# Kernel optimization log

Measured on AMD Instinct MI355X. Metric: run time of the kernel, lower is better.

The kernel has to match this reference:

```python
import jax, jax.numpy as jnp
import numpy as np

D_MODEL = 256   # per-head dim in this module
N_HEAD = 8
B, S = 4, 2048
NEG_INF = -1e9  # large negative in place of -inf for numerical safety


def setup_inputs() -> dict:
    key = jax.random.key(0)
    ks = jax.random.split(key, 8)
    d, h = D_MODEL, N_HEAD
    sc = 1.0 / np.sqrt(d)
    return {
        "Q": jax.random.normal(ks[0], (B, S, d), jnp.float32),
        "mask": jax.random.randint(ks[1], (B, S), 0, 2, jnp.int32),
        "WQ_w": jax.random.normal(ks[2], (h * d, d), jnp.float32) * sc,
        "WQ_b": jnp.zeros((h * d,), jnp.float32),
        "WK_w": jax.random.normal(ks[3], (h * d, d), jnp.float32) * sc,
        "WK_b": jnp.zeros((h * d,), jnp.float32),
        "WV_w": jax.random.normal(ks[4], (h * d, d), jnp.float32) * sc,
        "WV_b": jnp.zeros((h * d,), jnp.float32),
        "WO_w": jax.random.normal(ks[5], (d, h * d), jnp.float32) * sc,
        "WO_b": jnp.zeros((d,), jnp.float32),
        "ln_g": jnp.ones((d,), jnp.float32),
        "ln_b": jnp.zeros((d,), jnp.float32),
    }


def reference(Q, mask, WQ_w, WQ_b, WK_w, WK_b, WV_w, WV_b, WO_w, WO_b, ln_g, ln_b):
    b, s, d = Q.shape
    h = N_HEAD
    # projections (torch Linear: x @ W.T + b), split into heads: [b, h, s, d]
    q = (Q @ WQ_w.T + WQ_b).reshape(b, s, h, d).transpose(0, 2, 1, 3)
    k = (Q @ WK_w.T + WK_b).reshape(b, s, h, d).transpose(0, 2, 1, 3)
    v = (Q @ WV_w.T + WV_b).reshape(b, s, h, d).transpose(0, 2, 1, 3)
    # scaled dot-product scores [b, h, q, k]
    scores = jnp.einsum('bhqd,bhkd->bhqk', q, k) / jnp.sqrt(jnp.asarray(d, Q.dtype))
    key_mask = (mask != 0)[:, None, None, :]  # [b,1,1,k]
    scores = jnp.where(key_mask, scores, NEG_INF)
    alpha = jax.nn.softmax(scores, axis=-1)
    out = jnp.einsum('bhqk,bhkd->bhqd', alpha, v)
    out = out.transpose(0, 2, 1, 3).reshape(b, s, h * d)
    out = out @ WO_w.T + WO_b + Q  # dropout is identity in eval
    # LayerNorm over last dim
    mu = out.mean(-1, keepdims=True)
    var = out.var(-1, keepdims=True)
    return (out - mu) / jnp.sqrt(var + 1e-5) * ln_g + ln_b
```

## Files before the change

kernel.cpp:

```cpp
#include <hip/hip_runtime.h>
#include <cstddef>
#include <cstdint>

#define SQ 2048
#define DH 256
#define NH 8
#define BATCH 4
#define MROWS (BATCH*SQ)
#define HID (NH*DH)

typedef __attribute__((ext_vector_type(8)))  short bf16x8;
typedef __attribute__((ext_vector_type(16))) float f32x16;

typedef __attribute__((address_space(1))) const unsigned char gbuf_t;
typedef __attribute__((address_space(3))) unsigned char lbuf_t;

__device__ __forceinline__ void gl_lds16(const void* g, void* l) {
  __builtin_amdgcn_global_load_lds((gbuf_t*)g, (lbuf_t*)l, 16, 0, 0);
}

__device__ __forceinline__ unsigned short f2bf(float f) {
  unsigned u = __float_as_uint(f);
  unsigned r = (u + 0x7FFFu + ((u >> 16) & 1u)) >> 16;
  return (unsigned short)r;
}
__device__ __forceinline__ unsigned pk2(float a, float b) {
  return (unsigned)f2bf(a) | ((unsigned)f2bf(b) << 16);
}
__device__ __forceinline__ f32x16 zero16() {
  f32x16 v;
#pragma unroll
  for (int i = 0; i < 16; ++i) v[i] = 0.0f;
  return v;
}

__global__ void __launch_bounds__(256) cvt_kernel(
    const float* __restrict__ X,  const float* __restrict__ Wq,
    const float* __restrict__ Wk, const float* __restrict__ Wv,
    const float* __restrict__ Wo,
    unsigned short* __restrict__ Xb,  unsigned short* __restrict__ Wqb,
    unsigned short* __restrict__ Wkb, unsigned short* __restrict__ Wvb,
    unsigned short* __restrict__ Wob)
{
  int bid = blockIdx.x;
  const float* src; unsigned short* dst; size_t off;
  if      (bid < 512) { src = X;  dst = Xb;  off = (size_t)bid * 4096; }
  else if (bid < 640) { src = Wq; dst = Wqb; off = (size_t)(bid - 512) * 4096; }
  else if (bid < 768) { src = Wk; dst = Wkb; off = (size_t)(bid - 640) * 4096; }
  else if (bid < 896) { src = Wv; dst = Wvb; off = (size_t)(bid - 768) * 4096; }
  else                { src = Wo; dst = Wob; off = (size_t)(bid - 896) * 4096; }
  int tid = threadIdx.x;
#pragma unroll
  for (int k = 0; k < 4; ++k) {
    size_t idx = off + ((size_t)k * 256 + tid) * 4;
    float4 v = *(const float4*)(src + idx);
    uint2 o; o.x = pk2(v.x, v.y); o.y = pk2(v.z, v.w);
    *(uint2*)(dst + idx) = o;
  }
}

__global__ void __launch_bounds__(256) qkv_kernel(
    const unsigned short* __restrict__ Xbf,
    const unsigned short* __restrict__ Wqb,
    const unsigned short* __restrict__ Wkb,
    const unsigned short* __restrict__ Wvb,
    const float* __restrict__ bq, const float* __restrict__ bk, const float* __restrict__ bv,
    unsigned short* __restrict__ q_ws, unsigned short* __restrict__ k_ws,
    unsigned short* __restrict__ vt_ws)
{
  __shared__ unsigned char TA[65536];
  __shared__ unsigned char TB[65536];
  const int tid = threadIdx.x, w = tid >> 6, l = tid & 63;
  const int h = l >> 5, t = l & 31;
  const int wm = w >> 1, wn = w & 1;
  const int z = blockIdx.z;
  const int m0 = (z == 2) ? blockIdx.y * 128 : blockIdx.x * 128;
  const int n0 = (z == 2) ? blockIdx.x * 128 : blockIdx.y * 128;
  const unsigned short* Asrc = (z == 2) ? Wvb : Xbf;
  const unsigned short* Bsrc = (z == 0) ? Wqb : (z == 1) ? Wkb : Xbf;

  const int rowo = l >> 5;
  const int bin  = (l & 31) * 16;
#pragma unroll
  for (int i2 = 0; i2 < 16; ++i2) {
    int i = 16 * w + i2;
    int row = 2 * i + rowo;
    gl_lds16((const unsigned char*)(Asrc + (size_t)(m0 + row) * 256) + (bin ^ ((row & 15) << 4)),
             &TA[i * 1024]);
  }
#pragma unroll
  for (int i2 = 0; i2 < 16; ++i2) {
    int i = 16 * w + i2;
    int row = 2 * i + rowo;
    gl_lds16((const unsigned char*)(Bsrc + (size_t)(n0 + row) * 256) + (bin ^ ((row & 15) << 4)),
             &TB[i * 1024]);
  }
  __syncthreads();

  f32x16 acc00 = zero16(), acc01 = zero16(), acc10 = zero16(), acc11 = zero16();
  const int swz = (t & 15) << 4;
#pragma unroll
  for (int kc = 0; kc < 16; ++kc) {
    int kb = (32 * kc + 16 * h) ^ swz;
    bf16x8 a0 = *(const bf16x8*)&TA[(size_t)(64 * wm + t) * 512 + kb];
    bf16x8 a1 = *(const bf16x8*)&TA[(size_t)(64 * wm + 32 + t) * 512 + kb];
    bf16x8 b0 = *(const bf16x8*)&TB[(size_t)(64 * wn + t) * 512 + kb];
    bf16x8 b1 = *(const bf16x8*)&TB[(size_t)(64 * wn + 32 + t) * 512 + kb];
    acc00 = __builtin_amdgcn_mfma_f32_32x32x16_bf16(a0, b0, acc00, 0, 0, 0);
    acc01 = __builtin_amdgcn_mfma_f32_32x32x16_bf16(a0, b1, acc01, 0, 0, 0);
    acc10 = __builtin_amdgcn_mfma_f32_32x32x16_bf16(a1, b0, acc10, 0, 0, 0);
    acc11 = __builtin_amdgcn_mfma_f32_32x32x16_bf16(a1, b1, acc11, 0, 0, 0);
  }

  if (z < 2) {
    unsigned short* outp = z ? k_ws : q_ws;
    const float* bias = z ? bk : bq;
    float bn0 = bias[n0 + 64 * wn + t];
    float bn1 = bias[n0 + 64 * wn + 32 + t];
#pragma unroll
    for (int mt = 0; mt < 2; ++mt) {
#pragma unroll
      for (int nt = 0; nt < 2; ++nt) {
        int n = n0 + 64 * wn + 32 * nt + t;
        int headn = n >> 8, d = n & 255;
        float bb = nt ? bn1 : bn0;
        const f32x16& A = (mt == 0) ? (nt == 0 ? acc00 : acc01) : (nt == 0 ? acc10 : acc11);
#pragma unroll
        for (int r = 0; r < 16; ++r) {
          int m = m0 + 64 * wm + 32 * mt + (r & 3) + 8 * (r >> 2) + 4 * h;
          int batch = m >> 11, s = m & 2047;
          outp[(((size_t)batch * NH + headn) * SQ + s) * DH + d] = f2bf(A[r] + bb);
        }
      }
    }
  } else {
#pragma unroll
    for (int mt = 0; mt < 2; ++mt) {
#pragma unroll
      for (int r = 0; r < 16; ++r) {
        int j = m0 + 64 * wm + 32 * mt + (r & 3) + 8 * (r >> 2) + 4 * h;
        float bj = bv[j];
        int headj = j >> 8, jl = j & 255;
#pragma unroll
        for (int nt = 0; nt < 2; ++nt) {
          int sall = n0 + 64 * wn + 32 * nt + t;
          int batch = sall >> 11, ss = sall & 2047;
          const f32x16& A = (mt == 0) ? (nt == 0 ? acc00 : acc01) : (nt == 0 ? acc10 : acc11);
          vt_ws[((size_t)batch * NH + headj) * DH * SQ + (size_t)jl * SQ + ss] = f2bf(A[r] + bj);
        }
      }
    }
  }
}

__global__ void __launch_bounds__(512, 2) attn_kernel(
    const unsigned short* __restrict__ q_ws,
    const unsigned short* __restrict__ k_ws,
    const unsigned short* __restrict__ vt_ws,
    const int* __restrict__ mask,
    unsigned short* __restrict__ o_ws)
{
  __shared__ unsigned char KT[2][32768];
  __shared__ unsigned char VT[2][32768];
  __shared__ float MB[2048];

  const int tid = threadIdx.x, w = tid >> 6, l = tid & 63;
  const int h = l >> 5, t = l & 31;
  const int bid = blockIdx.x;
  const int xcd = bid & 7, slot = bid >> 3;
  const int bh = xcd * 4 + (slot >> 3);
  const int qt = slot & 7;
  const int b = bh >> 3, head = bh & 7;
  const int q0 = qt * 256;

  const float SC2 = 0.0625f * 1.44269504f;
  const float THR = 11.54f;

  {
    const int* mrow = mask + b * SQ;
    for (int i = tid; i < SQ; i += 512) MB[i] = mrow[i] ? 0.0f : -1.0e9f;
  }

  const unsigned short* kplane = k_ws + (size_t)bh * SQ * DH;
  const unsigned short* vplane = vt_ws + (size_t)bh * DH * SQ;

  bf16x8 qf[16];
  {
    const unsigned short* qb = q_ws + ((size_t)bh * SQ + (q0 + 32 * w + t)) * DH + 8 * h;
#pragma unroll
    for (int kc = 0; kc < 16; ++kc) qf[kc] = *(const bf16x8*)(qb + 16 * kc);
  }

  const int krow_o = l >> 5, kcol = (l & 31) * 16;
  const int vrow_o = l >> 3, vcol = (l & 7) * 16;

  {
#pragma unroll
    for (int i = 0; i < 4; ++i) {
      int j = 4 * w + i;
      int row = 2 * j + krow_o;
      gl_lds16((const unsigned char*)(kplane + (size_t)row * DH) + (kcol ^ ((row & 15) << 4)),
               &KT[0][j * 1024]);
    }
#pragma unroll
    for (int i = 0; i < 4; ++i) {
      int j = 4 * w + i;
      int row = 8 * j + vrow_o;
      gl_lds16((const unsigned char*)(vplane + (size_t)row * SQ) + (vcol ^ ((row & 7) << 4)),
               &VT[0][j * 1024]);
    }
  }
  __syncthreads();

  f32x16 o[8];
#pragma unroll
  for (int i = 0; i < 8; ++i) o[i] = zero16();
  float m_run = -3.0e38f, l_run = 0.0f;

  const int swzK = (t & 15) << 4;
  const int swzV = (t & 7) << 4;

  int cur = 0;
  for (int kb = 0; kb < SQ; kb += 64) {
    const int nxt = cur ^ 1;
    if (kb + 64 < SQ) {
#pragma unroll
      for (int i = 0; i < 4; ++i) {
        int j = 4 * w + i;
        int row = 2 * j + krow_o;
        gl_lds16((const unsigned char*)(kplane + (size_t)(kb + 64 + row) * DH) + (kcol ^ ((row & 15) << 4)),
                 &KT[nxt][j * 1024]);
      }
#pragma unroll
      for (int i = 0; i < 4; ++i) {
        int j = 4 * w + i;
        int row = 8 * j + vrow_o;
        gl_lds16((const unsigned char*)(vplane + (size_t)row * SQ + kb + 64) + (vcol ^ ((row & 7) << 4)),
                 &VT[nxt][j * 1024]);
      }
    }

    f32x16 sa0 = zero16(), sa1 = zero16();
    __builtin_amdgcn_s_setprio(1);
#pragma unroll
    for (int kc = 0; kc < 16; ++kc) {
      int kbb = (32 * kc + 16 * h) ^ swzK;
      bf16x8 a0 = *(const bf16x8*)&KT[cur][(size_t)t * 512 + kbb];
      bf16x8 a1 = *(const bf16x8*)&KT[cur][(size_t)(32 + t) * 512 + kbb];
      sa0 = __builtin_amdgcn_mfma_f32_32x32x16_bf16(a0, qf[kc], sa0, 0, 0, 0);
      sa1 = __builtin_amdgcn_mfma_f32_32x32x16_bf16(a1, qf[kc], sa1, 0, 0, 0);
    }
    __builtin_amdgcn_s_setprio(0);

    float tm = -3.0e38f;
#pragma unroll
    for (int g = 0; g < 4; ++g) {
      float4 m0v = *(const float4*)&MB[kb + 4 * h + 8 * g];
      float4 m1v = *(const float4*)&MB[kb + 32 + 4 * h + 8 * g];
      sa0[4*g+0] = sa0[4*g+0] * SC2 + m0v.x;
      sa0[4*g+1] = sa0[4*g+1] * SC2 + m0v.y;
      sa0[4*g+2] = sa0[4*g+2] * SC2 + m0v.z;
      sa0[4*g+3] = sa0[4*g+3] * SC2 + m0v.w;
      sa1[4*g+0] = sa1[4*g+0] * SC2 + m1v.x;
      sa1[4*g+1] = sa1[4*g+1] * SC2 + m1v.y;
      sa1[4*g+2] = sa1[4*g+2] * SC2 + m1v.z;
      sa1[4*g+3] = sa1[4*g+3] * SC2 + m1v.w;
      tm = fmaxf(tm, fmaxf(fmaxf(sa0[4*g+0], sa0[4*g+1]), fmaxf(sa0[4*g+2], sa0[4*g+3])));
      tm = fmaxf(tm, fmaxf(fmaxf(sa1[4*g+0], sa1[4*g+1]), fmaxf(sa1[4*g+2], sa1[4*g+3])));
    }
    tm = fmaxf(tm, __shfl_xor(tm, 32, 64));

    if (__builtin_expect(!__all(tm <= m_run + THR), 0)) {
      float m_new = fmaxf(m_run, tm);
      float rf = exp2f(m_run - m_new);
      m_run = m_new;
      l_run *= rf;
#pragma unroll
      for (int r = 0; r < 16; ++r) {
        float rr = __shfl(rf, (r & 3) + 8 * (r >> 2) + 4 * h, 64);
#pragma unroll
        for (int db = 0; db < 8; ++db) o[db][r] *= rr;
      }
    }

    float ls = 0.0f;
#pragma unroll
    for (int r = 0; r < 16; ++r) {
      sa0[r] = exp2f(sa0[r] - m_run);
      sa1[r] = exp2f(sa1[r] - m_run);
      ls += sa0[r] + sa1[r];
    }
    ls += __shfl_xor(ls, 32, 64);
    l_run += ls;

    bf16x8 pa[4];
#pragma unroll
    for (int ks = 0; ks < 4; ++ks) {
      const f32x16& P = (ks < 2) ? sa0 : sa1;
      const int base = 8 * (ks & 1);
      unsigned lo0, lo1, hi0, hi1;
      asm("v_cvt_pk_bf16_f32 %0, %1, %2" : "=v"(lo0) : "v"(P[base + 0]), "v"(P[base + 1]));
      asm("v_cvt_pk_bf16_f32 %0, %1, %2" : "=v"(lo1) : "v"(P[base + 2]), "v"(P[base + 3]));
      asm("v_cvt_pk_bf16_f32 %0, %1, %2" : "=v"(hi0) : "v"(P[base + 4]), "v"(P[base + 5]));
      asm("v_cvt_pk_bf16_f32 %0, %1, %2" : "=v"(hi1) : "v"(P[base + 6]), "v"(P[base + 7]));
      unsigned s0 = h ? lo0 : hi0;
      unsigned s1 = h ? lo1 : hi1;
      unsigned x0 = (unsigned)__shfl_xor((int)s0, 32, 64);
      unsigned x1 = (unsigned)__shfl_xor((int)s1, 32, 64);
      union { unsigned u[4]; bf16x8 v; } pu;
      pu.u[0] = h ? x0 : lo0;
      pu.u[1] = h ? x1 : lo1;
      pu.u[2] = h ? hi0 : x0;
      pu.u[3] = h ? hi1 : x1;
      pa[ks] = pu.v;
    }

    __builtin_amdgcn_s_setprio(1);
#pragma unroll
    for (int db = 0; db < 8; ++db) {
#pragma unroll
      for (int ks = 0; ks < 4; ++ks) {
        bf16x8 bv = *(const bf16x8*)&VT[cur][(size_t)(32 * db + t) * 128 + ((32 * ks + 16 * h) ^ swzV)];
        o[db] = __builtin_amdgcn_mfma_f32_32x32x16_bf16(pa[ks], bv, o[db], 0, 0, 0);
      }
    }
    __builtin_amdgcn_s_setprio(0);

    __syncthreads();
    cur = nxt;
  }

  float linv = 1.0f / l_run;
  unsigned short* ob = o_ws + (size_t)b * SQ * HID + (size_t)head * DH;
#pragma unroll
  for (int r = 0; r < 16; ++r) {
    int rowr = (r & 3) + 8 * (r >> 2) + 4 * h;
    float li = __shfl(linv, rowr, 64);
    int s = q0 + 32 * w + rowr;
    unsigned short* orow = ob + (size_t)s * HID;
#pragma unroll
    for (int db = 0; db < 8; ++db)
      orow[32 * db + t] = f2bf(o[db][r] * li);
  }
}

__global__ void __launch_bounds__(256) oproj_kernel(
    const unsigned short* __restrict__ Abf,
    const unsigned short* __restrict__ Wob,
    float* __restrict__ tmp)
{
  __shared__ unsigned char TA[8192];
  __shared__ unsigned char TB[16384];
  const int tid = threadIdx.x, w = tid >> 6, l = tid & 63;
  const int h = l >> 5, t = l & 31;
  const int wm = w >> 1, wn = w & 1;
  const int m0 = blockIdx.x * 64, n0 = blockIdx.y * 128;
  const int arow_o = l >> 3, ab_in = (l & 7) * 16;
  const int swz = (t & 7) << 4;

  f32x16 acc0 = zero16(), acc1 = zero16();
  for (int chunk = 0; chunk < 32; ++chunk) {
    __syncthreads();
#pragma unroll
    for (int i2 = 0; i2 < 2; ++i2) {
      int i = 2 * w + i2;
      int row = 8 * i + arow_o;
      gl_lds16((const unsigned char*)(Abf + (size_t)(m0 + row) * HID + chunk * 64) + (ab_in ^ ((row & 7) << 4)),
               &TA[i * 1024]);
    }
#pragma unroll
    for (int i2 = 0; i2 < 4; ++i2) {
      int i = 4 * w + i2;
      int row = 8 * i + arow_o;
      gl_lds16((const unsigned char*)(Wob + (size_t)(n0 + row) * HID + chunk * 64) + (ab_in ^ ((row & 7) << 4)),
               &TB[i * 1024]);
    }
    __syncthreads();
#pragma unroll
    for (int kc = 0; kc < 4; ++kc) {
      int kbb = (32 * kc + 16 * h) ^ swz;
      bf16x8 a  = *(const bf16x8*)&TA[(size_t)(32 * wm + t) * 128 + kbb];
      bf16x8 b0 = *(const bf16x8*)&TB[(size_t)(64 * wn + t) * 128 + kbb];
      bf16x8 b1 = *(const bf16x8*)&TB[(size_t)(64 * wn + 32 + t) * 128 + kbb];
      acc0 = __builtin_amdgcn_mfma_f32_32x32x16_bf16(a, b0, acc0, 0, 0, 0);
      acc1 = __builtin_amdgcn_mfma_f32_32x32x16_bf16(a, b1, acc1, 0, 0, 0);
    }
  }
#pragma unroll
  for (int nt = 0; nt < 2; ++nt) {
    const f32x16& A = nt ? acc1 : acc0;
    int n = n0 + 64 * wn + 32 * nt + t;
#pragma unroll
    for (int r = 0; r < 16; ++r) {
      int m = m0 + 32 * wm + (r & 3) + 8 * (r >> 2) + 4 * h;
      tmp[(size_t)m * DH + n] = A[r];
    }
  }
}

__global__ void __launch_bounds__(256) ln_kernel(
    const float* __restrict__ tmp, const float* __restrict__ bo,
    const float* __restrict__ Xin, const float* __restrict__ g,
    const float* __restrict__ be, float* __restrict__ out)
{
  const int tid = threadIdx.x, w = tid >> 6, lane = tid & 63;
  const int row = blockIdx.x * 4 + w;
  float4 v  = ((const float4*)(tmp + (size_t)row * DH))[lane];
  float4 qv = ((const float4*)(Xin + (size_t)row * DH))[lane];
  float4 bb = ((const float4*)bo)[lane];
  v.x += qv.x + bb.x; v.y += qv.y + bb.y; v.z += qv.z + bb.z; v.w += qv.w + bb.w;
  float s1 = v.x + v.y + v.z + v.w;
  float s2 = v.x * v.x + v.y * v.y + v.z * v.z + v.w * v.w;
#pragma unroll
  for (int off = 1; off < 64; off <<= 1) {
    s1 += __shfl_xor(s1, off, 64);
    s2 += __shfl_xor(s2, off, 64);
  }
  float mean = s1 * (1.0f / 256.0f);
  float var = s2 * (1.0f / 256.0f) - mean * mean;
  float rstd = rsqrtf(var + 1e-5f);
  float4 gg = ((const float4*)g)[lane];
  float4 b2 = ((const float4*)be)[lane];
  float4 o;
  o.x = (v.x - mean) * rstd * gg.x + b2.x;
  o.y = (v.y - mean) * rstd * gg.y + b2.y;
  o.z = (v.z - mean) * rstd * gg.z + b2.z;
  o.w = (v.w - mean) * rstd * gg.w + b2.w;
  ((float4*)(out + (size_t)row * DH))[lane] = o;
}

extern "C" void kernel_launch(void* const* d_in, const int* in_sizes, int n_in,
                              void* d_out, int out_size, void* d_ws, size_t ws_size,
                              hipStream_t stream) {
  const float* Q    = (const float*)d_in[0];
  const int*   mask = (const int*)  d_in[1];
  const float* WQ_w = (const float*)d_in[2];
  const float* WQ_b = (const float*)d_in[3];
  const float* WK_w = (const float*)d_in[4];
  const float* WK_b = (const float*)d_in[5];
  const float* WV_w = (const float*)d_in[6];
  const float* WV_b = (const float*)d_in[7];
  const float* WO_w = (const float*)d_in[8];
  const float* WO_b = (const float*)d_in[9];
  const float* ln_g = (const float*)d_in[10];
  const float* ln_b = (const float*)d_in[11];
  float* out = (float*)d_out;

  uint8_t* ws = (uint8_t*)d_ws;
  const size_t MB1 = 1048576;
  unsigned short* Xb   = (unsigned short*)(ws + 0 * MB1);
  unsigned short* Wqb  = (unsigned short*)(ws + 4 * MB1);
  unsigned short* Wkb  = (unsigned short*)(ws + 5 * MB1);
  unsigned short* Wvb  = (unsigned short*)(ws + 6 * MB1);
  unsigned short* Wob  = (unsigned short*)(ws + 7 * MB1);
  unsigned short* q_ws = (unsigned short*)(ws + 8 * MB1);
  unsigned short* k_ws = (unsigned short*)(ws + 40 * MB1);
  unsigned short* vtws = (unsigned short*)(ws + 72 * MB1);
  unsigned short* o_ws = (unsigned short*)(ws + 104 * MB1);
  float*          tmpf = (float*)         (ws + 136 * MB1);

  cvt_kernel<<<1024, 256, 0, stream>>>(Q, WQ_w, WK_w, WV_w, WO_w, Xb, Wqb, Wkb, Wvb, Wob);
  qkv_kernel<<<dim3(64, 16, 3), 256, 0, stream>>>(Xb, Wqb, Wkb, Wvb, WQ_b, WK_b, WV_b,
                                                  q_ws, k_ws, vtws);
  attn_kernel<<<dim3(256), 512, 0, stream>>>(q_ws, k_ws, vtws, mask, o_ws);
  oproj_kernel<<<dim3(128, 2), 256, 0, stream>>>(o_ws, Wob, tmpf);
  ln_kernel<<<2048, 256, 0, stream>>>(tmpf, WO_b, Q, ln_g, ln_b, out);
}
```

Before: 313.0 us.

## Load K and V fragments directly from global memory instead of LDS staging

```diff
diff --git a/kernel.cpp b/kernel.cpp
--- a/kernel.cpp
+++ b/kernel.cpp
@@ -160,8 +160,6 @@
     const int* __restrict__ mask,
     unsigned short* __restrict__ o_ws)
 {
-  __shared__ unsigned char KT[2][32768];
-  __shared__ unsigned char VT[2][32768];
   __shared__ float MB[2048];
 
   const int tid = threadIdx.x, w = tid >> 6, l = tid & 63;
@@ -180,6 +178,7 @@
     const int* mrow = mask + b * SQ;
     for (int i = tid; i < SQ; i += 512) MB[i] = mrow[i] ? 0.0f : -1.0e9f;
   }
+  __syncthreads();
 
   const unsigned short* kplane = k_ws + (size_t)bh * SQ * DH;
   const unsigned short* vplane = vt_ws + (size_t)bh * DH * SQ;
@@ -191,62 +190,20 @@
     for (int kc = 0; kc < 16; ++kc) qf[kc] = *(const bf16x8*)(qb + 16 * kc);
   }
 
-  const int krow_o = l >> 5, kcol = (l & 31) * 16;
-  const int vrow_o = l >> 3, vcol = (l & 7) * 16;
-
-  {
-#pragma unroll
-    for (int i = 0; i < 4; ++i) {
-      int j = 4 * w + i;
-      int row = 2 * j + krow_o;
-      gl_lds16((const unsigned char*)(kplane + (size_t)row * DH) + (kcol ^ ((row & 15) << 4)),
-               &KT[0][j * 1024]);
-    }
-#pragma unroll
-    for (int i = 0; i < 4; ++i) {
-      int j = 4 * w + i;
-      int row = 8 * j + vrow_o;
-      gl_lds16((const unsigned char*)(vplane + (size_t)row * SQ) + (vcol ^ ((row & 7) << 4)),
-               &VT[0][j * 1024]);
-    }
-  }
-  __syncthreads();
-
   f32x16 o[8];
 #pragma unroll
   for (int i = 0; i < 8; ++i) o[i] = zero16();
   float m_run = -3.0e38f, l_run = 0.0f;
 
-  const int swzK = (t & 15) << 4;
-  const int swzV = (t & 7) << 4;
-
-  int cur = 0;
   for (int kb = 0; kb < SQ; kb += 64) {
-    const int nxt = cur ^ 1;
-    if (kb + 64 < SQ) {
-#pragma unroll
-      for (int i = 0; i < 4; ++i) {
-        int j = 4 * w + i;
-        int row = 2 * j + krow_o;
-        gl_lds16((const unsigned char*)(kplane + (size_t)(kb + 64 + row) * DH) + (kcol ^ ((row & 15) << 4)),
-                 &KT[nxt][j * 1024]);
-      }
-#pragma unroll
-      for (int i = 0; i < 4; ++i) {
-        int j = 4 * w + i;
-        int row = 8 * j + vrow_o;
-        gl_lds16((const unsigned char*)(vplane + (size_t)row * SQ + kb + 64) + (vcol ^ ((row & 7) << 4)),
-                 &VT[nxt][j * 1024]);
-      }
-    }
-
+    const unsigned short* ka0 = kplane + (size_t)(kb + t) * DH + 8 * h;
+    const unsigned short* ka1 = kplane + (size_t)(kb + 32 + t) * DH + 8 * h;
     f32x16 sa0 = zero16(), sa1 = zero16();
     __builtin_amdgcn_s_setprio(1);
 #pragma unroll
     for (int kc = 0; kc < 16; ++kc) {
-      int kbb = (32 * kc + 16 * h) ^ swzK;
-      bf16x8 a0 = *(const bf16x8*)&KT[cur][(size_t)t * 512 + kbb];
-      bf16x8 a1 = *(const bf16x8*)&KT[cur][(size_t)(32 + t) * 512 + kbb];
+      bf16x8 a0 = *(const bf16x8*)(ka0 + 16 * kc);
+      bf16x8 a1 = *(const bf16x8*)(ka1 + 16 * kc);
       sa0 = __builtin_amdgcn_mfma_f32_32x32x16_bf16(a0, qf[kc], sa0, 0, 0, 0);
       sa1 = __builtin_amdgcn_mfma_f32_32x32x16_bf16(a1, qf[kc], sa1, 0, 0, 0);
     }
@@ -318,16 +275,14 @@
     __builtin_amdgcn_s_setprio(1);
 #pragma unroll
     for (int db = 0; db < 8; ++db) {
+      const unsigned short* vb = vplane + (size_t)(32 * db + t) * SQ + kb + 8 * h;
 #pragma unroll
       for (int ks = 0; ks < 4; ++ks) {
-        bf16x8 bv = *(const bf16x8*)&VT[cur][(size_t)(32 * db + t) * 128 + ((32 * ks + 16 * h) ^ swzV)];
+        bf16x8 bv = *(const bf16x8*)(vb + 16 * ks);
         o[db] = __builtin_amdgcn_mfma_f32_32x32x16_bf16(pa[ks], bv, o[db], 0, 0, 0);
       }
     }
     __builtin_amdgcn_s_setprio(0);
-
-    __syncthreads();
-    cur = nxt;
   }
 
   float linv = 1.0f / l_run;
```

Result: slower. 618.3 us (+97.5%).
